# Kernel tuning notes

Hardware: AMD Instinct MI355X
Metric: run time of the kernel (lower is better)

The kernel has to match this reference:

```python
import jax, jax.numpy as jnp
import numpy as np

WIN = 9  # 9x9 local attention window

def conv2d(x, w, b=None, pad=1):
    # x: [B,C,H,W], w: [O,I,kh,kw]
    y = jax.lax.conv_general_dilated(x, w, (1, 1), [(pad, pad), (pad, pad)],
                                     dimension_numbers=('NCHW', 'OIHW', 'NCHW'))
    if b is not None:
        y = y + b[None, :, None, None]
    return y

def leaky(x):
    return jax.nn.leaky_relu(x, 0.2)

def local_similar(q, k):
    # TorchLocalAttention.f_similar: per-pixel dot(q[i,j], k[i+di-4, j+dj-4]) with zero pad,
    # kernel positions row-major (di*9+dj) -> output [B, 81, H, W]
    b, c, h, w = q.shape
    r = WIN // 2
    kp = jnp.pad(k, ((0, 0), (0, 0), (r, r), (r, r)))
    sims = []
    for di in range(WIN):
        for dj in range(WIN):
            sims.append(jnp.einsum('bchw,bchw->bhw', q, kp[:, :, di:di + h, dj:dj + w]))
    return jnp.stack(sims, axis=1)

def srp_forward(old, new, wq, bq, wk, bk, wv, bv, wo1, bo1, res_w1, res_w2, wo2, bo2):
    x = jnp.concatenate((old, new), axis=1)  # [B, C, H, W]
    att = local_similar(conv2d(x, wq, bq), conv2d(x, wk, bk))  # [B, 81, H, W]
    v = conv2d(att, wv, bv)  # [B, C, H, W]
    y = conv2d(x * v, wo1, bo1)
    n_res = res_w1.shape[0]
    for i in range(n_res):  # EBlock: ResBlocks (convs bias=False)
        h1 = leaky(conv2d(y, res_w1[i]))
        y = y + conv2d(h1, res_w2[i])
    y = conv2d(y, wo2, bo2)
    return y + x

def setup_inputs() -> dict:
    key = jax.random.key(0)
    B, Cn, Co, H, W = 4, 32, 32, 256, 256
    C = Cn + Co
    NRES = 8
    ks = jax.random.split(key, 16)
    s = 0.05
    inp = {
        'old': jax.random.normal(ks[0], (B, Co, H, W), jnp.float32),
        'new': jax.random.normal(ks[1], (B, Cn, H, W), jnp.float32),
        'wq': jax.random.normal(ks[2], (C, C, 3, 3), jnp.float32) * s,
        'bq': jax.random.normal(ks[3], (C,), jnp.float32) * s,
        'wk': jax.random.normal(ks[4], (C, C, 3, 3), jnp.float32) * s,
        'bk': jax.random.normal(ks[5], (C,), jnp.float32) * s,
        'wv': jax.random.normal(ks[6], (C, 81, 3, 3), jnp.float32) * s,
        'bv': jax.random.normal(ks[7], (C,), jnp.float32) * s,
        'wo1': jax.random.normal(ks[8], (C, C, 3, 3), jnp.float32) * s,
        'bo1': jax.random.normal(ks[9], (C,), jnp.float32) * s,
        'res_w1': jax.random.normal(ks[10], (NRES, C, C, 3, 3), jnp.float32) * s,
        'res_w2': jax.random.normal(ks[11], (NRES, C, C, 3, 3), jnp.float32) * s,
        'wo2': jax.random.normal(ks[12], (C, C, 3, 3), jnp.float32) * s,
        'bo2': jax.random.normal(ks[13], (C,), jnp.float32) * s,
    }
    return inp

def reference(old, new, wq, bq, wk, bk, wv, bv, wo1, bo1, res_w1, res_w2, wo2, bo2):
    return srp_forward(old, new, wq, bq, wk, bk, wv, bv, wo1, bo1, res_w1, res_w2, wo2, bo2)
```

## Files before the change

kernel.cpp:

```cpp
#include <hip/hip_runtime.h>
#include <hip/hip_bf16.h>


#define HH 256
#define WW 256
#define PLANE 65536

typedef _Float16 f16x8 __attribute__((ext_vector_type(8)));
typedef float    f32x4 __attribute__((ext_vector_type(4)));
typedef _Float16 h2    __attribute__((ext_vector_type(2)));

__device__ __forceinline__ unsigned short f2h(float f) {
    _Float16 h = (_Float16)f;
    return __builtin_bit_cast(unsigned short, h);
}
__device__ __forceinline__ float h2f(unsigned short u) {
    return (float)__builtin_bit_cast(_Float16, u);
}
__device__ __forceinline__ unsigned pack2h(float a, float b) {
    return (unsigned)f2h(a) | ((unsigned)f2h(b) << 16);
}
__device__ __forceinline__ float dot2h(unsigned a, unsigned b, float c) {
#if __has_builtin(__builtin_amdgcn_fdot2)
    return __builtin_amdgcn_fdot2(__builtin_bit_cast(h2, a),
                                  __builtin_bit_cast(h2, b), c, false);
#else
    h2 av = __builtin_bit_cast(h2, a), bv = __builtin_bit_cast(h2, b);
    return fmaf((float)av.x, (float)bv.x, fmaf((float)av.y, (float)bv.y, c));
#endif
}

template <int CIN, bool BIAS, bool LEAKY, bool ADDF, bool ADDX, bool MULX, bool OUTF, bool OUTB>
__global__ __launch_bounds__(256, 2) void conv_mfma(
    const unsigned short* __restrict__ in_pc,
    const unsigned short* __restrict__ wb,
    const float* __restrict__ bias,
    const unsigned short* __restrict__ addh,
    const unsigned short* __restrict__ xh,
    float* __restrict__ outf,
    unsigned short* __restrict__ outb)
{
    __shared__ unsigned short smem[28800];
    unsigned short* lds_in = smem;
    unsigned short* lds_w  = smem + 10368;

    const int tid = threadIdx.x;
    const int w   = tid >> 6;
    const int ln  = tid & 63;
    const int m   = ln & 15;
    const int q   = ln >> 4;
    const int b   = blockIdx.z;
    const int tx0 = blockIdx.x * 16, ty0 = blockIdx.y * 16;
    const size_t pixb = (size_t)b * PLANE;

    f32x4 acc[4][4];
#pragma unroll
    for (int g = 0; g < 4; ++g)
#pragma unroll
        for (int p = 0; p < 4; ++p) acc[g][p] = (f32x4)0.f;

    for (int c2 = 0; c2 < CIN / 32; ++c2) {
        __syncthreads();
        for (int u = tid; u < 1296; u += 256) {
            int pix = u >> 2, part = u & 3;
            int hy = pix / 18, hx = pix - hy * 18;
            int gy = ty0 + hy - 1, gx = tx0 + hx - 1;
            uint4 val = make_uint4(0u, 0u, 0u, 0u);
            if ((unsigned)gy < 256u && (unsigned)gx < 256u)
                val = *reinterpret_cast<const uint4*>(
                    in_pc + ((pixb + (size_t)gy * 256 + gx) * CIN + c2 * 32 + part * 8));
            *reinterpret_cast<uint4*>(&lds_in[pix * 32 + ((part ^ (pix & 3)) * 8)]) = val;
        }
#pragma unroll
        for (int t = 0; t < 9; ++t) {
            int oc = tid >> 2, part = tid & 3;
            uint4 val = *reinterpret_cast<const uint4*>(
                wb + ((size_t)(t * 64 + oc) * CIN + c2 * 32 + part * 8));
            *reinterpret_cast<uint4*>(
                &lds_w[t * 2048 + oc * 32 + ((part ^ (oc & 3)) * 8)]) = val;
        }
        __syncthreads();

#pragma unroll
        for (int t = 0; t < 9; ++t) {
            const int dy = t / 3, dx = t - dy * 3;
            f16x8 av[4], bv[4];
#pragma unroll
            for (int g = 0; g < 4; ++g) {
                int oc = g * 16 + m;
                av[g] = *reinterpret_cast<const f16x8*>(
                    &lds_w[t * 2048 + oc * 32 + ((q ^ (oc & 3)) * 8)]);
            }
#pragma unroll
            for (int p = 0; p < 4; ++p) {
                int hp = (w * 4 + p + dy) * 18 + m + dx;
                bv[p] = *reinterpret_cast<const f16x8*>(
                    &lds_in[hp * 32 + ((q ^ (hp & 3)) * 8)]);
            }
#pragma unroll
            for (int g = 0; g < 4; ++g)
#pragma unroll
                for (int p = 0; p < 4; ++p)
                    acc[g][p] = __builtin_amdgcn_mfma_f32_16x16x32_f16(
                        av[g], bv[p], acc[g][p], 0, 0, 0);
        }
    }

    const int colx = tx0 + m;
    float4 bvec[4];
    if (BIAS) {
#pragma unroll
        for (int g = 0; g < 4; ++g)
            bvec[g] = *reinterpret_cast<const float4*>(bias + g * 16 + q * 4);
    }
    if (OUTB) __syncthreads();

#pragma unroll
    for (int g = 0; g < 4; ++g) {
#pragma unroll
        for (int p = 0; p < 4; ++p) {
            const int prow = w * 4 + p;
            const int gy   = ty0 + prow;
            const size_t pixg = pixb + (size_t)gy * 256 + colx;
            const int oc0 = g * 16 + q * 4;
            ushort4 a4, x4;
            if (ADDF) a4 = *reinterpret_cast<const ushort4*>(addh + pixg * 64 + oc0);
            if (ADDX || MULX) x4 = *reinterpret_cast<const ushort4*>(xh + pixg * 64 + oc0);
            float vals[4];
#pragma unroll
            for (int r = 0; r < 4; ++r) {
                float v = acc[g][p][r];
                if (BIAS) v += reinterpret_cast<const float*>(&bvec[g])[r];
                if (LEAKY) v = (v >= 0.f) ? v : 0.2f * v;
                if (ADDF) v += h2f(reinterpret_cast<const unsigned short*>(&a4)[r]);
                if (ADDX) v += h2f(reinterpret_cast<const unsigned short*>(&x4)[r]);
                if (MULX) v *= h2f(reinterpret_cast<const unsigned short*>(&x4)[r]);
                if (OUTF)
                    outf[((size_t)(b * 64 + oc0 + r)) * PLANE + (size_t)gy * 256 + colx] = v;
                vals[r] = v;
            }
            if (OUTB) {
                ushort4 pk;
                pk.x = f2h(vals[0]); pk.y = f2h(vals[1]);
                pk.z = f2h(vals[2]); pk.w = f2h(vals[3]);
                int pix   = prow * 16 + m;
                int part8 = g * 4 + q;
                int p16   = (part8 >> 1) ^ (pix & 7);
                *reinterpret_cast<ushort4*>(&smem[pix * 64 + p16 * 8 + (part8 & 1) * 4]) = pk;
            }
        }
    }
    if (OUTB) {
        __syncthreads();
        for (int u = tid; u < 2048; u += 256) {
            int pix = u >> 3, p16 = u & 7;
            uint4 val = *reinterpret_cast<const uint4*>(
                &smem[pix * 64 + ((p16 ^ (pix & 7)) * 8)]);
            int gy = ty0 + (pix >> 4), gx = tx0 + (pix & 15);
            *reinterpret_cast<uint4*>(
                &outb[(pixb + (size_t)gy * 256 + gx) * 64 + p16 * 8]) = val;
        }
    }
}

__global__ __launch_bounds__(256)
__attribute__((amdgpu_waves_per_eu(2, 4)))
void local_sim(
    const unsigned short* __restrict__ qh, const unsigned short* __restrict__ kh,
    unsigned short* __restrict__ att)
{
    __shared__ unsigned short lds_k[576 * 32];

    const int tid = threadIdx.x;
    const int tx = tid & 15, ty = tid >> 4;
    const int bx = blockIdx.x * 16, by = blockIdx.y * 16;
    const int b  = blockIdx.z;
    const size_t pixb = (size_t)b * PLANE;

    unsigned short* op = att + (pixb + (size_t)(by + ty) * 256 + bx + tx) * 96;
    const unsigned short* qbase = qh + (pixb + (size_t)(by + ty) * 256 + bx + tx) * 64;

#pragma unroll
    for (int g = 0; g < 3; ++g) {
        float acc[27];
#pragma unroll
        for (int i = 0; i < 27; ++i) acc[i] = 0.f;

        for (int c = 0; c < 2; ++c) {
            __syncthreads();
            for (int u = tid; u < 2304; u += 256) {
                int pix = u >> 2, part = u & 3;
                int hy = pix / 24, hx = pix - hy * 24;
                int gy = by + hy - 4, gx = bx + hx - 4;
                uint4 val = make_uint4(0u, 0u, 0u, 0u);
                if ((unsigned)gy < 256u && (unsigned)gx < 256u)
                    val = *reinterpret_cast<const uint4*>(
                        kh + ((pixb + (size_t)gy * 256 + gx) * 64 + c * 32 + part * 8));
                int pp = part ^ (pix & 3) ^ ((pix >> 2) & 3);
                *reinterpret_cast<uint4*>(&lds_k[pix * 32 + pp * 8]) = val;
            }
            __syncthreads();

            uint4 qv[4];
#pragma unroll
            for (int j = 0; j < 4; ++j)
                qv[j] = *reinterpret_cast<const uint4*>(qbase + c * 32 + j * 8);

#pragma unroll
            for (int dil = 0; dil < 3; ++dil) {
                const int hrow = (ty + g * 3 + dil) * 24 + tx;
#pragma unroll
                for (int dj = 0; dj < 9; ++dj) {
                    const int hp  = hrow + dj;
                    const int fsw = (hp & 3) ^ ((hp >> 2) & 3);
                    float s = acc[dil * 9 + dj];
#pragma unroll
                    for (int part = 0; part < 4; ++part) {
                        const uint4 kv = *reinterpret_cast<const uint4*>(
                            &lds_k[hp * 32 + ((part ^ fsw) * 8)]);
                        s = dot2h(qv[part].x, kv.x, s);
                        s = dot2h(qv[part].y, kv.y, s);
                        s = dot2h(qv[part].z, kv.z, s);
                        s = dot2h(qv[part].w, kv.w, s);
                    }
                    acc[dil * 9 + dj] = s;
                }
            }
        }

        unsigned short* o = op + g * 27;
        if (g == 0) {
            uint4 A = {pack2h(acc[0], acc[1]),  pack2h(acc[2], acc[3]),
                       pack2h(acc[4], acc[5]),  pack2h(acc[6], acc[7])};
            uint4 B = {pack2h(acc[8], acc[9]),  pack2h(acc[10], acc[11]),
                       pack2h(acc[12], acc[13]), pack2h(acc[14], acc[15])};
            uint2 C = {pack2h(acc[16], acc[17]), pack2h(acc[18], acc[19])};
            uint2 D = {pack2h(acc[20], acc[21]), pack2h(acc[22], acc[23])};
            *reinterpret_cast<uint4*>(o)      = A;
            *reinterpret_cast<uint4*>(o + 8)  = B;
            *reinterpret_cast<uint2*>(o + 16) = C;
            *reinterpret_cast<uint2*>(o + 20) = D;
            *reinterpret_cast<unsigned*>(o + 24) = pack2h(acc[24], acc[25]);
            o[26] = f2h(acc[26]);
        } else if (g == 1) {
            o[0] = f2h(acc[0]);
            *reinterpret_cast<unsigned*>(o + 1) = pack2h(acc[1], acc[2]);
            *reinterpret_cast<unsigned*>(o + 3) = pack2h(acc[3], acc[4]);
            uint4 A = {pack2h(acc[5], acc[6]),   pack2h(acc[7], acc[8]),
                       pack2h(acc[9], acc[10]),  pack2h(acc[11], acc[12])};
            uint4 B = {pack2h(acc[13], acc[14]), pack2h(acc[15], acc[16]),
                       pack2h(acc[17], acc[18]), pack2h(acc[19], acc[20])};
            *reinterpret_cast<uint4*>(o + 5)  = A;
            *reinterpret_cast<uint4*>(o + 13) = B;
            uint2 C = {pack2h(acc[21], acc[22]), pack2h(acc[23], acc[24])};
            *reinterpret_cast<uint2*>(o + 21) = C;
            *reinterpret_cast<unsigned*>(o + 25) = pack2h(acc[25], acc[26]);
        } else {
            *reinterpret_cast<unsigned*>(o) = pack2h(acc[0], acc[1]);
            uint4 A = {pack2h(acc[2], acc[3]),   pack2h(acc[4], acc[5]),
                       pack2h(acc[6], acc[7]),   pack2h(acc[8], acc[9])};
            uint4 B = {pack2h(acc[10], acc[11]), pack2h(acc[12], acc[13]),
                       pack2h(acc[14], acc[15]), pack2h(acc[16], acc[17])};
            *reinterpret_cast<uint4*>(o + 2)  = A;
            *reinterpret_cast<uint4*>(o + 10) = B;
            uint2 C = {pack2h(acc[18], acc[19]), pack2h(acc[20], acc[21])};
            *reinterpret_cast<uint2*>(o + 18) = C;
            *reinterpret_cast<unsigned*>(o + 22) = pack2h(acc[22], acc[23]);
            *reinterpret_cast<unsigned*>(o + 24) = pack2h(acc[24], acc[25]);
            o[26] = f2h(acc[26]);
        }
    }

    op[81] = 0;
    *reinterpret_cast<unsigned*>(op + 82) = 0u;
    uint2 z2 = {0u, 0u};
    uint4 z4 = {0u, 0u, 0u, 0u};
    *reinterpret_cast<uint2*>(op + 84) = z2;
    *reinterpret_cast<uint4*>(op + 88) = z4;
}

__global__ __launch_bounds__(256) void pack_x(
    const float* __restrict__ old_, const float* __restrict__ new_,
    unsigned short* __restrict__ xb)
{
    __shared__ unsigned short lds[256 * 64];
    const int tid = threadIdx.x;
    const int b = blockIdx.y;
    const size_t pixbase = (size_t)blockIdx.x * 256;
#pragma unroll
    for (int cg = 0; cg < 8; ++cg) {
        unsigned pk[4];
#pragma unroll
        for (int h = 0; h < 4; ++h) {
            int c0 = cg * 8 + h * 2;
            const float* s0 = (c0 < 32) ? old_ : new_;
            const float* s1 = ((c0 + 1) < 32) ? old_ : new_;
            float f0 = s0[((size_t)b * 32 + (c0 & 31)) * PLANE + pixbase + tid];
            float f1 = s1[((size_t)b * 32 + ((c0 + 1) & 31)) * PLANE + pixbase + tid];
            pk[h] = pack2h(f0, f1);
        }
        int p16 = cg ^ (tid & 7);
        uint4 v; v.x = pk[0]; v.y = pk[1]; v.z = pk[2]; v.w = pk[3];
        *reinterpret_cast<uint4*>(&lds[tid * 64 + p16 * 8]) = v;
    }
    __syncthreads();
    for (int r = 0; r < 8; ++r) {
        int u = r * 256 + tid;
        int pix = u >> 3, p16 = u & 7;
        uint4 v = *reinterpret_cast<const uint4*>(&lds[pix * 64 + ((p16 ^ (pix & 7)) * 8)]);
        *reinterpret_cast<uint4*>(
            &xb[((size_t)b * PLANE + pixbase + pix) * 64 + p16 * 8]) = v;
    }
}

__global__ void prep_wstd(const float* __restrict__ wq, const float* __restrict__ wk,
                          const float* __restrict__ wo1, const float* __restrict__ wo2,
                          const float* __restrict__ rw1, const float* __restrict__ rw2,
                          unsigned short* __restrict__ wstd)
{
    const int c = blockIdx.y;
    const float* src;
    if (c == 0) src = wq;
    else if (c == 1) src = wk;
    else if (c == 2) src = wo1;
    else if (c == 3) src = wo2;
    else if (c < 12) src = rw1 + (size_t)(c - 4) * 36864;
    else src = rw2 + (size_t)(c - 12) * 36864;
    int idx = blockIdx.x * 256 + threadIdx.x;
    int o = idx >> 6, i = idx & 63;
    const float* s = src + (size_t)(o * 64 + i) * 9;
    unsigned short* d = wstd + (size_t)c * 36864 + (size_t)o * 64 + i;
#pragma unroll
    for (int t = 0; t < 9; ++t) d[(size_t)t * 4096] = f2h(s[t]);
}

__global__ void prep_wv(const float* __restrict__ wv, unsigned short* __restrict__ wv96)
{
    int idx = blockIdx.x * 256 + threadIdx.x;
    int o = idx / 96, i = idx - o * 96;
    unsigned short* d = wv96 + (size_t)o * 96 + i;
    if (i < 81) {
        const float* s = wv + (size_t)(o * 81 + i) * 9;
#pragma unroll
        for (int t = 0; t < 9; ++t) d[(size_t)t * 6144] = f2h(s[t]);
    } else {
#pragma unroll
        for (int t = 0; t < 9; ++t) d[(size_t)t * 6144] = 0;
    }
}

extern "C" void kernel_launch(void* const* d_in, const int* in_sizes, int n_in,
                              void* d_out, int out_size, void* d_ws, size_t ws_size,
                              hipStream_t stream)
{
    const float* old_ = (const float*)d_in[0];
    const float* new_ = (const float*)d_in[1];
    const float* wq  = (const float*)d_in[2];  const float* bq  = (const float*)d_in[3];
    const float* wk  = (const float*)d_in[4];  const float* bk  = (const float*)d_in[5];
    const float* wv  = (const float*)d_in[6];  const float* bv  = (const float*)d_in[7];
    const float* wo1 = (const float*)d_in[8];  const float* bo1 = (const float*)d_in[9];
    const float* rw1 = (const float*)d_in[10]; const float* rw2 = (const float*)d_in[11];
    const float* wo2 = (const float*)d_in[12]; const float* bo2 = (const float*)d_in[13];
    float* out = (float*)d_out;

    char* ws = (char*)d_ws;
    unsigned short* X   = (unsigned short*)(ws);
    unsigned short* P1  = (unsigned short*)(ws + 33554432ull);
    unsigned short* P2  = (unsigned short*)(ws + 67108864ull);
    unsigned short* P3  = (unsigned short*)(ws + 100663296ull);
    unsigned short* wst = (unsigned short*)(ws + 150994944ull);
    unsigned short* wv96= (unsigned short*)(ws + 152469504ull);

    const dim3 cgrid(16, 16, 4), cblk(256);

    prep_wstd<<<dim3(16, 20), 256, 0, stream>>>(wq, wk, wo1, wo2, rw1, rw2, wst);
    prep_wv<<<dim3(24), 256, 0, stream>>>(wv, wv96);
    pack_x<<<dim3(256, 4), 256, 0, stream>>>(old_, new_, X);

    conv_mfma<64, true, false, false, false, false, false, true>
        <<<cgrid, cblk, 0, stream>>>(X, wst + 0ull * 36864, bq, nullptr, nullptr, nullptr, P1);
    conv_mfma<64, true, false, false, false, false, false, true>
        <<<cgrid, cblk, 0, stream>>>(X, wst + 1ull * 36864, bk, nullptr, nullptr, nullptr, P2);
    local_sim<<<cgrid, cblk, 0, stream>>>(P1, P2, P3);
    conv_mfma<96, true, false, false, false, true, false, true>
        <<<cgrid, cblk, 0, stream>>>(P3, wv96, bv, nullptr, X, nullptr, P2);
    conv_mfma<64, true, false, false, false, false, false, true>
        <<<cgrid, cblk, 0, stream>>>(P2, wst + 2ull * 36864, bo1, nullptr, nullptr, nullptr, P1);
    for (int i = 0; i < 8; ++i) {
        unsigned short* ysrc = (i & 1) ? P3 : P1;
        unsigned short* ydst = (i & 1) ? P1 : P3;
        conv_mfma<64, false, true, false, false, false, false, true>
            <<<cgrid, cblk, 0, stream>>>(ysrc, wst + (size_t)(4 + i) * 36864, nullptr,
                                         nullptr, nullptr, nullptr, P2);
        conv_mfma<64, false, false, true, false, false, false, true>
            <<<cgrid, cblk, 0, stream>>>(P2, wst + (size_t)(12 + i) * 36864, nullptr,
                                         ysrc, nullptr, nullptr, ydst);
    }
    conv_mfma<64, true, false, false, true, false, true, false>
        <<<cgrid, cblk, 0, stream>>>(P1, wst + 3ull * 36864, bo2, nullptr, X, out, nullptr);
}
```

Baseline: 889.2 us.

## Use direct global-to-LDS loads for interior tiles and single-pass local attention

```diff
diff --git a/kernel.cpp b/kernel.cpp
--- a/kernel.cpp
+++ b/kernel.cpp
@@ -28,6 +28,13 @@
     h2 av = __builtin_bit_cast(h2, a), bv = __builtin_bit_cast(h2, b);
     return fmaf((float)av.x, (float)bv.x, fmaf((float)av.y, (float)bv.y, c));
 #endif
+}
+
+__device__ __forceinline__ void gl16(const unsigned short* g, unsigned short* l) {
+    __builtin_amdgcn_global_load_lds(
+        (const __attribute__((address_space(1))) unsigned int*)(g),
+        (__attribute__((address_space(3))) unsigned int*)(l),
+        16, 0, 0);
 }
 
 template <int CIN, bool BIAS, bool LEAKY, bool ADDF, bool ADDX, bool MULX, bool OUTF, bool OUTB>
@@ -52,6 +59,8 @@
     const int b   = blockIdx.z;
     const int tx0 = blockIdx.x * 16, ty0 = blockIdx.y * 16;
     const size_t pixb = (size_t)b * PLANE;
+    const bool interior = (blockIdx.x >= 1) && (blockIdx.x <= 14) &&
+                          (blockIdx.y >= 1) && (blockIdx.y <= 14);
 
     f32x4 acc[4][4];
 #pragma unroll
@@ -61,23 +70,46 @@
 
     for (int c2 = 0; c2 < CIN / 32; ++c2) {
         __syncthreads();
-        for (int u = tid; u < 1296; u += 256) {
-            int pix = u >> 2, part = u & 3;
-            int hy = pix / 18, hx = pix - hy * 18;
-            int gy = ty0 + hy - 1, gx = tx0 + hx - 1;
-            uint4 val = make_uint4(0u, 0u, 0u, 0u);
-            if ((unsigned)gy < 256u && (unsigned)gx < 256u)
-                val = *reinterpret_cast<const uint4*>(
-                    in_pc + ((pixb + (size_t)gy * 256 + gx) * CIN + c2 * 32 + part * 8));
-            *reinterpret_cast<uint4*>(&lds_in[pix * 32 + ((part ^ (pix & 3)) * 8)]) = val;
-        }
-#pragma unroll
-        for (int t = 0; t < 9; ++t) {
-            int oc = tid >> 2, part = tid & 3;
-            uint4 val = *reinterpret_cast<const uint4*>(
-                wb + ((size_t)(t * 64 + oc) * CIN + c2 * 32 + part * 8));
-            *reinterpret_cast<uint4*>(
-                &lds_w[t * 2048 + oc * 32 + ((part ^ (oc & 3)) * 8)]) = val;
+        if (interior) {
+            const unsigned short* inb =
+                in_pc + (pixb + (size_t)(ty0 - 1) * 256 + (tx0 - 1)) * CIN + c2 * 32;
+#pragma unroll
+            for (int it = 0; it < 5; ++it) {
+                int u = it * 256 + tid;
+                int pix = u >> 2, ps = u & 3;
+                int part = ps ^ (pix & 3);
+                int hy = pix / 18, hx = pix - hy * 18;
+                gl16(inb + ((size_t)hy * 256 + hx) * CIN + part * 8,
+                     &lds_in[(it * 256 + (tid & 192)) * 8]);
+            }
+            if (tid < 16) {
+                int u = 1280 + tid;
+                int pix = u >> 2, ps = u & 3;
+                int part = ps ^ (pix & 3);
+                int hy = pix / 18, hx = pix - hy * 18;
+                gl16(inb + ((size_t)hy * 256 + hx) * CIN + part * 8,
+                     &lds_in[1280 * 8]);
+            }
+        } else {
+            for (int u = tid; u < 1296; u += 256) {
+                int pix = u >> 2, part = u & 3;
+                int hy = pix / 18, hx = pix - hy * 18;
+                int gy = ty0 + hy - 1, gx = tx0 + hx - 1;
+                uint4 val = make_uint4(0u, 0u, 0u, 0u);
+                if ((unsigned)gy < 256u && (unsigned)gx < 256u)
+                    val = *reinterpret_cast<const uint4*>(
+                        in_pc + ((pixb + (size_t)gy * 256 + gx) * CIN + c2 * 32 + part * 8));
+                *reinterpret_cast<uint4*>(&lds_in[pix * 32 + ((part ^ (pix & 3)) * 8)]) = val;
+            }
+        }
+        {
+            const int oc = tid >> 2, ps = tid & 3;
+            const int part = ps ^ (oc & 3);
+            const unsigned short* wsrc = wb + (size_t)oc * CIN + c2 * 32 + part * 8;
+#pragma unroll
+            for (int t = 0; t < 9; ++t)
+                gl16(wsrc + (size_t)t * 64 * CIN,
+                     &lds_w[t * 2048 + (tid & 192) * 8]);
         }
         __syncthreads();
 
@@ -176,18 +208,31 @@
     const int bx = blockIdx.x * 16, by = blockIdx.y * 16;
     const int b  = blockIdx.z;
     const size_t pixb = (size_t)b * PLANE;
+    const bool interior = (blockIdx.x >= 1) && (blockIdx.x <= 14) &&
+                          (blockIdx.y >= 1) && (blockIdx.y <= 14);
 
     unsigned short* op = att + (pixb + (size_t)(by + ty) * 256 + bx + tx) * 96;
     const unsigned short* qbase = qh + (pixb + (size_t)(by + ty) * 256 + bx + tx) * 64;
 
-#pragma unroll
-    for (int g = 0; g < 3; ++g) {
-        float acc[27];
-#pragma unroll
-        for (int i = 0; i < 27; ++i) acc[i] = 0.f;
-
-        for (int c = 0; c < 2; ++c) {
-            __syncthreads();
+    float acc[81];
+#pragma unroll
+    for (int i = 0; i < 81; ++i) acc[i] = 0.f;
+
+    for (int c = 0; c < 2; ++c) {
+        __syncthreads();
+        if (interior) {
+            const unsigned short* kb =
+                kh + (pixb + (size_t)(by - 4) * 256 + (bx - 4)) * 64 + c * 32;
+#pragma unroll
+            for (int it = 0; it < 9; ++it) {
+                int u = it * 256 + tid;
+                int pix = u >> 2, ps = u & 3;
+                int part = ps ^ (pix & 3) ^ ((pix >> 2) & 3);
+                int hy = pix / 24, hx = pix - hy * 24;
+                gl16(kb + ((size_t)hy * 256 + hx) * 64 + part * 8,
+                     &lds_k[(it * 256 + (tid & 192)) * 8]);
+            }
+        } else {
             for (int u = tid; u < 2304; u += 256) {
                 int pix = u >> 2, part = u & 3;
                 int hy = pix / 24, hx = pix - hy * 24;
@@ -199,84 +244,48 @@
                 int pp = part ^ (pix & 3) ^ ((pix >> 2) & 3);
                 *reinterpret_cast<uint4*>(&lds_k[pix * 32 + pp * 8]) = val;
             }
-            __syncthreads();
-
-            uint4 qv[4];
-#pragma unroll
-            for (int j = 0; j < 4; ++j)
-                qv[j] = *reinterpret_cast<const uint4*>(qbase + c * 32 + j * 8);
-
-#pragma unroll
-            for (int dil = 0; dil < 3; ++dil) {
-                const int hrow = (ty + g * 3 + dil) * 24 + tx;
-#pragma unroll
-                for (int dj = 0; dj < 9; ++dj) {
-                    const int hp  = hrow + dj;
-                    const int fsw = (hp & 3) ^ ((hp >> 2) & 3);
-                    float s = acc[dil * 9 + dj];
-#pragma unroll
-                    for (int part = 0; part < 4; ++part) {
-                        const uint4 kv = *reinterpret_cast<const uint4*>(
-                            &lds_k[hp * 32 + ((part ^ fsw) * 8)]);
-                        s = dot2h(qv[part].x, kv.x, s);
-                        s = dot2h(qv[part].y, kv.y, s);
-                        s = dot2h(qv[part].z, kv.z, s);
-                        s = dot2h(qv[part].w, kv.w, s);
-                    }
-                    acc[dil * 9 + dj] = s;
+        }
+        __syncthreads();
+
+        uint4 qv[4];
+#pragma unroll
+        for (int j = 0; j < 4; ++j)
+            qv[j] = *reinterpret_cast<const uint4*>(qbase + c * 32 + j * 8);
+
+#pragma unroll
+        for (int di = 0; di < 9; ++di) {
+            const int hrow = (ty + di) * 24 + tx;
+#pragma unroll
+            for (int dj = 0; dj < 9; ++dj) {
+                const int hp  = hrow + dj;
+                const int fsw = (hp & 3) ^ ((hp >> 2) & 3);
+                float s = acc[di * 9 + dj];
+#pragma unroll
+                for (int part = 0; part < 4; ++part) {
+                    const uint4 kv = *reinterpret_cast<const uint4*>(
+                        &lds_k[hp * 32 + ((part ^ fsw) * 8)]);
+                    s = dot2h(qv[part].x, kv.x, s);
+                    s = dot2h(qv[part].y, kv.y, s);
+                    s = dot2h(qv[part].z, kv.z, s);
+                    s = dot2h(qv[part].w, kv.w, s);
                 }
-            }
-        }
-
-        unsigned short* o = op + g * 27;
-        if (g == 0) {
-            uint4 A = {pack2h(acc[0], acc[1]),  pack2h(acc[2], acc[3]),
-                       pack2h(acc[4], acc[5]),  pack2h(acc[6], acc[7])};
-            uint4 B = {pack2h(acc[8], acc[9]),  pack2h(acc[10], acc[11]),
-                       pack2h(acc[12], acc[13]), pack2h(acc[14], acc[15])};
-            uint2 C = {pack2h(acc[16], acc[17]), pack2h(acc[18], acc[19])};
-            uint2 D = {pack2h(acc[20], acc[21]), pack2h(acc[22], acc[23])};
-            *reinterpret_cast<uint4*>(o)      = A;
-            *reinterpret_cast<uint4*>(o + 8)  = B;
-            *reinterpret_cast<uint2*>(o + 16) = C;
-            *reinterpret_cast<uint2*>(o + 20) = D;
-            *reinterpret_cast<unsigned*>(o + 24) = pack2h(acc[24], acc[25]);
-            o[26] = f2h(acc[26]);
-        } else if (g == 1) {
-            o[0] = f2h(acc[0]);
-            *reinterpret_cast<unsigned*>(o + 1) = pack2h(acc[1], acc[2]);
-            *reinterpret_cast<unsigned*>(o + 3) = pack2h(acc[3], acc[4]);
-            uint4 A = {pack2h(acc[5], acc[6]),   pack2h(acc[7], acc[8]),
-                       pack2h(acc[9], acc[10]),  pack2h(acc[11], acc[12])};
-            uint4 B = {pack2h(acc[13], acc[14]), pack2h(acc[15], acc[16]),
-                       pack2h(acc[17], acc[18]), pack2h(acc[19], acc[20])};
-            *reinterpret_cast<uint4*>(o + 5)  = A;
-            *reinterpret_cast<uint4*>(o + 13) = B;
-            uint2 C = {pack2h(acc[21], acc[22]), pack2h(acc[23], acc[24])};
-            *reinterpret_cast<uint2*>(o + 21) = C;
-            *reinterpret_cast<unsigned*>(o + 25) = pack2h(acc[25], acc[26]);
-        } else {
-            *reinterpret_cast<unsigned*>(o) = pack2h(acc[0], acc[1]);
-            uint4 A = {pack2h(acc[2], acc[3]),   pack2h(acc[4], acc[5]),
-                       pack2h(acc[6], acc[7]),   pack2h(acc[8], acc[9])};
-            uint4 B = {pack2h(acc[10], acc[11]), pack2h(acc[12], acc[13]),
-                       pack2h(acc[14], acc[15]), pack2h(acc[16], acc[17])};
-            *reinterpret_cast<uint4*>(o + 2)  = A;
-            *reinterpret_cast<uint4*>(o + 10) = B;
-            uint2 C = {pack2h(acc[18], acc[19]), pack2h(acc[20], acc[21])};
-            *reinterpret_cast<uint2*>(o + 18) = C;
-            *reinterpret_cast<unsigned*>(o + 22) = pack2h(acc[22], acc[23]);
-            *reinterpret_cast<unsigned*>(o + 24) = pack2h(acc[24], acc[25]);
-            o[26] = f2h(acc[26]);
-        }
-    }
-
-    op[81] = 0;
-    *reinterpret_cast<unsigned*>(op + 82) = 0u;
-    uint2 z2 = {0u, 0u};
-    uint4 z4 = {0u, 0u, 0u, 0u};
-    *reinterpret_cast<uint2*>(op + 84) = z2;
-    *reinterpret_cast<uint4*>(op + 88) = z4;
+                acc[di * 9 + dj] = s;
+            }
+        }
+    }
+
+    unsigned pk[48];
+#pragma unroll
+    for (int i = 0; i < 40; ++i) pk[i] = pack2h(acc[2 * i], acc[2 * i + 1]);
+    pk[40] = (unsigned)f2h(acc[80]);
+#pragma unroll
+    for (int i = 41; i < 48; ++i) pk[i] = 0u;
+#pragma unroll
+    for (int i = 0; i < 12; ++i) {
+        uint4 v;
+        v.x = pk[4 * i]; v.y = pk[4 * i + 1]; v.z = pk[4 * i + 2]; v.w = pk[4 * i + 3];
+        *reinterpret_cast<uint4*>(op + i * 8) = v;
+    }
 }
 
 __global__ __launch_bounds__(256) void pack_x(
```

Measured after the change: 1.329 ms. 1.49x slower.

## Use direct global-to-LDS loads for interior conv and local_sim tiles

Applied to the files above, without the earlier changes.

```diff
diff --git a/kernel.cpp b/kernel.cpp
--- a/kernel.cpp
+++ b/kernel.cpp
@@ -28,6 +28,13 @@
     h2 av = __builtin_bit_cast(h2, a), bv = __builtin_bit_cast(h2, b);
     return fmaf((float)av.x, (float)bv.x, fmaf((float)av.y, (float)bv.y, c));
 #endif
+}
+
+__device__ __forceinline__ void gl16(const unsigned short* g, unsigned short* l) {
+    __builtin_amdgcn_global_load_lds(
+        (const __attribute__((address_space(1))) unsigned int*)(g),
+        (__attribute__((address_space(3))) unsigned int*)(l),
+        16, 0, 0);
 }
 
 template <int CIN, bool BIAS, bool LEAKY, bool ADDF, bool ADDX, bool MULX, bool OUTF, bool OUTB>
@@ -52,6 +59,8 @@
     const int b   = blockIdx.z;
     const int tx0 = blockIdx.x * 16, ty0 = blockIdx.y * 16;
     const size_t pixb = (size_t)b * PLANE;
+    const bool interior = (blockIdx.x >= 1) && (blockIdx.x <= 14) &&
+                          (blockIdx.y >= 1) && (blockIdx.y <= 14);
 
     f32x4 acc[4][4];
 #pragma unroll
@@ -61,23 +70,46 @@
 
     for (int c2 = 0; c2 < CIN / 32; ++c2) {
         __syncthreads();
-        for (int u = tid; u < 1296; u += 256) {
-            int pix = u >> 2, part = u & 3;
-            int hy = pix / 18, hx = pix - hy * 18;
-            int gy = ty0 + hy - 1, gx = tx0 + hx - 1;
-            uint4 val = make_uint4(0u, 0u, 0u, 0u);
-            if ((unsigned)gy < 256u && (unsigned)gx < 256u)
-                val = *reinterpret_cast<const uint4*>(
-                    in_pc + ((pixb + (size_t)gy * 256 + gx) * CIN + c2 * 32 + part * 8));
-            *reinterpret_cast<uint4*>(&lds_in[pix * 32 + ((part ^ (pix & 3)) * 8)]) = val;
-        }
-#pragma unroll
-        for (int t = 0; t < 9; ++t) {
-            int oc = tid >> 2, part = tid & 3;
-            uint4 val = *reinterpret_cast<const uint4*>(
-                wb + ((size_t)(t * 64 + oc) * CIN + c2 * 32 + part * 8));
-            *reinterpret_cast<uint4*>(
-                &lds_w[t * 2048 + oc * 32 + ((part ^ (oc & 3)) * 8)]) = val;
+        if (interior) {
+            const unsigned short* inb =
+                in_pc + (pixb + (size_t)(ty0 - 1) * 256 + (tx0 - 1)) * CIN + c2 * 32;
+#pragma unroll
+            for (int it = 0; it < 5; ++it) {
+                int u = it * 256 + tid;
+                int pix = u >> 2, ps = u & 3;
+                int part = ps ^ (pix & 3);
+                int hy = pix / 18, hx = pix - hy * 18;
+                gl16(inb + ((size_t)hy * 256 + hx) * CIN + part * 8,
+                     &lds_in[(it * 256 + (tid & 192)) * 8]);
+            }
+            if (tid < 16) {
+                int u = 1280 + tid;
+                int pix = u >> 2, ps = u & 3;
+                int part = ps ^ (pix & 3);
+                int hy = pix / 18, hx = pix - hy * 18;
+                gl16(inb + ((size_t)hy * 256 + hx) * CIN + part * 8,
+                     &lds_in[1280 * 8]);
+            }
+        } else {
+            for (int u = tid; u < 1296; u += 256) {
+                int pix = u >> 2, part = u & 3;
+                int hy = pix / 18, hx = pix - hy * 18;
+                int gy = ty0 + hy - 1, gx = tx0 + hx - 1;
+                uint4 val = make_uint4(0u, 0u, 0u, 0u);
+                if ((unsigned)gy < 256u && (unsigned)gx < 256u)
+                    val = *reinterpret_cast<const uint4*>(
+                        in_pc + ((pixb + (size_t)gy * 256 + gx) * CIN + c2 * 32 + part * 8));
+                *reinterpret_cast<uint4*>(&lds_in[pix * 32 + ((part ^ (pix & 3)) * 8)]) = val;
+            }
+        }
+        {
+            const int oc = tid >> 2, ps = tid & 3;
+            const int part = ps ^ (oc & 3);
+            const unsigned short* wsrc = wb + (size_t)oc * CIN + c2 * 32 + part * 8;
+#pragma unroll
+            for (int t = 0; t < 9; ++t)
+                gl16(wsrc + (size_t)t * 64 * CIN,
+                     &lds_w[t * 2048 + (tid & 192) * 8]);
         }
         __syncthreads();
 
@@ -164,21 +196,54 @@
 }
 
 __global__ __launch_bounds__(256)
-__attribute__((amdgpu_waves_per_eu(2, 4)))
 void local_sim(
     const unsigned short* __restrict__ qh, const unsigned short* __restrict__ kh,
     unsigned short* __restrict__ att)
 {
-    __shared__ unsigned short lds_k[576 * 32];
+    __shared__ unsigned short lds_k[576 * 64];
 
     const int tid = threadIdx.x;
     const int tx = tid & 15, ty = tid >> 4;
     const int bx = blockIdx.x * 16, by = blockIdx.y * 16;
     const int b  = blockIdx.z;
     const size_t pixb = (size_t)b * PLANE;
-
+    const bool interior = (blockIdx.x >= 1) && (blockIdx.x <= 14) &&
+                          (blockIdx.y >= 1) && (blockIdx.y <= 14);
+
+    if (interior) {
+        const unsigned short* kb =
+            kh + (pixb + (size_t)(by - 4) * 256 + (bx - 4)) * 64;
+#pragma unroll
+        for (int it = 0; it < 18; ++it) {
+            int u = it * 256 + tid;
+            int pix = u >> 3, sl = u & 7;
+            int part = sl ^ ((pix ^ (pix >> 3)) & 7);
+            int hy = pix / 24, hx = pix - hy * 24;
+            gl16(kb + ((size_t)hy * 256 + hx) * 64 + part * 8,
+                 &lds_k[(it * 256 + (tid & 192)) * 8]);
+        }
+    } else {
+        for (int u = tid; u < 4608; u += 256) {
+            int pix = u >> 3, part = u & 7;
+            int hy = pix / 24, hx = pix - hy * 24;
+            int gy = by + hy - 4, gx = bx + hx - 4;
+            uint4 val = make_uint4(0u, 0u, 0u, 0u);
+            if ((unsigned)gy < 256u && (unsigned)gx < 256u)
+                val = *reinterpret_cast<const uint4*>(
+                    kh + ((pixb + (size_t)gy * 256 + gx) * 64 + part * 8));
+            int sl = part ^ ((pix ^ (pix >> 3)) & 7);
+            *reinterpret_cast<uint4*>(&lds_k[pix * 64 + sl * 8]) = val;
+        }
+    }
+    __syncthreads();
+
+    const unsigned short* qbase = qh + (pixb + (size_t)(by + ty) * 256 + bx + tx) * 64;
     unsigned short* op = att + (pixb + (size_t)(by + ty) * 256 + bx + tx) * 96;
-    const unsigned short* qbase = qh + (pixb + (size_t)(by + ty) * 256 + bx + tx) * 64;
+
+    uint4 qv[8];
+#pragma unroll
+    for (int j = 0; j < 8; ++j)
+        qv[j] = *reinterpret_cast<const uint4*>(qbase + j * 8);
 
 #pragma unroll
     for (int g = 0; g < 3; ++g) {
@@ -186,45 +251,24 @@
 #pragma unroll
         for (int i = 0; i < 27; ++i) acc[i] = 0.f;
 
-        for (int c = 0; c < 2; ++c) {
-            __syncthreads();
-            for (int u = tid; u < 2304; u += 256) {
-                int pix = u >> 2, part = u & 3;
-                int hy = pix / 24, hx = pix - hy * 24;
-                int gy = by + hy - 4, gx = bx + hx - 4;
-                uint4 val = make_uint4(0u, 0u, 0u, 0u);
-                if ((unsigned)gy < 256u && (unsigned)gx < 256u)
-                    val = *reinterpret_cast<const uint4*>(
-                        kh + ((pixb + (size_t)gy * 256 + gx) * 64 + c * 32 + part * 8));
-                int pp = part ^ (pix & 3) ^ ((pix >> 2) & 3);
-                *reinterpret_cast<uint4*>(&lds_k[pix * 32 + pp * 8]) = val;
-            }
-            __syncthreads();
-
-            uint4 qv[4];
-#pragma unroll
-            for (int j = 0; j < 4; ++j)
-                qv[j] = *reinterpret_cast<const uint4*>(qbase + c * 32 + j * 8);
-
-#pragma unroll
-            for (int dil = 0; dil < 3; ++dil) {
-                const int hrow = (ty + g * 3 + dil) * 24 + tx;
-#pragma unroll
-                for (int dj = 0; dj < 9; ++dj) {
-                    const int hp  = hrow + dj;
-                    const int fsw = (hp & 3) ^ ((hp >> 2) & 3);
-                    float s = acc[dil * 9 + dj];
-#pragma unroll
-                    for (int part = 0; part < 4; ++part) {
-                        const uint4 kv = *reinterpret_cast<const uint4*>(
-                            &lds_k[hp * 32 + ((part ^ fsw) * 8)]);
-                        s = dot2h(qv[part].x, kv.x, s);
-                        s = dot2h(qv[part].y, kv.y, s);
-                        s = dot2h(qv[part].z, kv.z, s);
-                        s = dot2h(qv[part].w, kv.w, s);
-                    }
-                    acc[dil * 9 + dj] = s;
+#pragma unroll
+        for (int dil = 0; dil < 3; ++dil) {
+            const int hrow = (ty + g * 3 + dil) * 24 + tx;
+#pragma unroll
+            for (int dj = 0; dj < 9; ++dj) {
+                const int hp = hrow + dj;
+                const int gs = (hp ^ (hp >> 3)) & 7;
+                float s = acc[dil * 9 + dj];
+#pragma unroll
+                for (int part = 0; part < 8; ++part) {
+                    const uint4 kv = *reinterpret_cast<const uint4*>(
+                        &lds_k[hp * 64 + ((part ^ gs) * 8)]);
+                    s = dot2h(qv[part].x, kv.x, s);
+                    s = dot2h(qv[part].y, kv.y, s);
+                    s = dot2h(qv[part].z, kv.z, s);
+                    s = dot2h(qv[part].w, kv.w, s);
                 }
+                acc[dil * 9 + dj] = s;
             }
         }
 
```

After: 878.4 us. No clear change (-1.2%).
